# Kernel optimization log

Measured on AMD Instinct MI355X. Metric: run time of the kernel, lower is better.

Reference implementation:

```python
import jax, jax.numpy as jnp
import numpy as np

B, S, H, HEAD = 4, 4096, 512, 128
GAMMA = 0.96875
SCALE_BASE = 512  # XPOS default scale_base


def rotate_every_two(x):
    # (..., d) -> interleave (-x2, x1) pairs, matching torch stack+flatten
    x1 = x[..., ::2]
    x2 = x[..., 1::2]
    return jnp.stack((-x2, x1), axis=-1).reshape(x.shape)


def duplicate_interleave(m):
    # (L, d/2) -> (L, d): each column repeated twice, interleaved
    return jnp.repeat(m, 2, axis=-1)


def xpos(x, downscale=False):
    # x: (B, L, d). Faithful to XPOS module with offset=0.
    L, d = x.shape[1], x.shape[2]
    half = d // 2
    base_scale = (jnp.arange(0, d, 2, dtype=jnp.float32) + 0.4 * d) / (1.4 * d)  # (half,)
    power = jnp.arange(L, dtype=jnp.float32)[:, None] / SCALE_BASE              # (L,1)
    scale = base_scale[None, :] ** power                                        # (L,half)
    inv_freq = 1.0 / (10000.0 ** (jnp.arange(half, dtype=jnp.float32) / half))  # (half,)
    sinusoid = jnp.arange(L, dtype=jnp.float32)[:, None] * inv_freq[None, :]    # (L,half)
    sin, cos = jnp.sin(sinusoid), jnp.cos(sinusoid)
    if downscale:
        scale = 1.0 / scale
    sin = duplicate_interleave(sin * scale)  # (L,d)
    cos = duplicate_interleave(cos * scale)  # (L,d)
    return x * cos[None] + rotate_every_two(x) * sin[None]


def decay_mask(s1, s2, gamma):
    n = jnp.arange(s1)[:, None]
    m = jnp.arange(s2)[None, :]
    keep = n >= m
    # guard exponent to avoid inf for n<m (original zeroes NaNs from inf*0)
    exp = jnp.where(keep, (n - m).astype(jnp.float32), 0.0)
    return jnp.where(keep, gamma ** exp, 0.0)  # (s1,s2)


def setup_inputs() -> dict:
    key = jax.random.key(0)
    k1, k2, k3, k4, k5 = jax.random.split(key, 5)
    return {
        "X": jax.random.normal(k1, (B, S, H), dtype=jnp.float32),
        "Mem": jax.random.normal(k2, (B, S, H), dtype=jnp.float32),
        "W_Q": jax.random.normal(k3, (H, HEAD), dtype=jnp.float32) / H,
        "W_K": jax.random.normal(k4, (H, HEAD), dtype=jnp.float32) / H,
        "W_V": jax.random.normal(k5, (H, HEAD), dtype=jnp.float32) / H,
    }


def reference(X, Mem, W_Q, W_K, W_V):
    s1, s2 = X.shape[1], Mem.shape[1]
    D = decay_mask(s1, s2, GAMMA)                 # (s1,s2)
    Q = xpos(X @ W_Q)                              # (B,s1,head)
    K = xpos(Mem @ W_K, downscale=True)            # (B,s2,head)
    V = Mem @ W_V                                  # (B,s2,v)
    ret = jnp.einsum("bnd,bmd->bnm", Q, K) * D[None]  # (B,s1,s2)
    return ret @ V                                 # (B,s1,v)
```

## Files before the change

### kernel.cpp

```cpp
#include <hip/hip_runtime.h>
#include <hip/hip_bf16.h>

#define S_LEN 4096
#define HID   512
#define HD    128
#define LOG2_GAMMA (-0.0458036933f)

typedef short bf16x8 __attribute__((ext_vector_type(8)));
typedef float f32x4  __attribute__((ext_vector_type(4)));
typedef unsigned short u16;

static __device__ __forceinline__ u16 f2bf(float f) {
    union { float f; unsigned u; } v; v.f = f;
    unsigned r = (v.u + 0x7fffu + ((v.u >> 16) & 1u)) >> 16;
    return (u16)r;
}

static __device__ __forceinline__ unsigned pk2(float lo, float hi) {
    __hip_bfloat162 h = __float22bfloat162_rn(make_float2(lo, hi));
    union { __hip_bfloat162 h; unsigned u; } c; c.h = h; return c.u;
}
static __device__ __forceinline__ bf16x8 pack8(float4 a, float4 b) {
    union { unsigned u[4]; bf16x8 v; } r;
    r.u[0] = pk2(a.x, a.y); r.u[1] = pk2(a.z, a.w);
    r.u[2] = pk2(b.x, b.y); r.u[3] = pk2(b.z, b.w);
    return r.v;
}

static __device__ __forceinline__ void gload16(const void* g, void* l) {
    __builtin_amdgcn_global_load_lds(
        (const __attribute__((address_space(1))) unsigned*)g,
        (__attribute__((address_space(3))) unsigned*)l, 16, 0, 0);
}

__global__ __launch_bounds__(256) void prep_kernel(const float* __restrict__ WQ,
                                                   const float* __restrict__ WK,
                                                   const float* __restrict__ WV,
                                                   u16* __restrict__ Wt,
                                                   float2* __restrict__ tabQ,
                                                   float2* __restrict__ tabK) {
    if (blockIdx.x < 1024) {
        int idx = blockIdx.x * 256 + threadIdx.x;
        int n = idx >> 6, i = idx & 63;
        float base  = (2.0f * i + 51.2f) * (1.0f / 179.2f);
        float power = (float)n * (1.0f / 512.0f);
        float scale = exp2f(power * log2f(base));
        float inv_freq = exp2f(-(float)i * (13.287712379549449f / 64.0f));
        float theta = (float)n * inv_freq;
        float s, c;
        sincosf(theta, &s, &c);
        tabQ[idx] = make_float2(c * scale, s * scale);
        float is = 1.0f / scale;
        tabK[idx] = make_float2(c * is, s * is);
    } else {
        int idx = (blockIdx.x - 1024) * 256 + threadIdx.x;
        int w = idx >> 16;
        int rem = idx & 65535;
        int c = rem >> 9, k = rem & 511;
        const float* src = (w == 0) ? WQ : (w == 1) ? WK : WV;
        Wt[idx] = f2bf(src[k * HD + c]);
    }
}

__global__ __launch_bounds__(256) void proj_kernel(const float* __restrict__ X,
                                                   const float* __restrict__ Mem,
                                                   const u16* __restrict__ Wt,
                                                   const float2* __restrict__ tabQ,
                                                   const float2* __restrict__ tabK,
                                                   u16* __restrict__ Qo,
                                                   u16* __restrict__ Ko,
                                                   u16* __restrict__ Vt) {
    __shared__ __align__(16) float A_lds[2][2048];
    __shared__ __align__(16) u16   B_lds[2][2][4096];
    const int tid  = threadIdx.x;
    const int wave = tid >> 6, lane = tid & 63;
    const int l15  = lane & 15, quad = lane >> 4;
    const int rt_base = blockIdx.x * 64;

    if (blockIdx.y == 0) {
        auto stage = [&](int ch, int p) {
            const int kc0 = ch * 32;
#pragma unroll
            for (int i = 0; i < 2; ++i) {
                int L = i * 256 + tid;
                int row = L >> 3;
                int s = (L & 7) ^ (row & 7);
                gload16(X + (size_t)(rt_base + row) * HID + kc0 + s * 4,
                        &A_lds[p][(i * 256 + wave * 64) * 4]);
            }
#pragma unroll
            for (int i = 0; i < 2; ++i) {
                int L = i * 256 + tid;
                int col = L >> 2;
                int s = (L & 3) ^ ((col >> 1) & 3);
                gload16(Wt + (size_t)col * HID + kc0 + s * 8,
                        &B_lds[p][0][(i * 256 + wave * 64) * 8]);
            }
        };

        f32x4 acc[8];
#pragma unroll
        for (int ct = 0; ct < 8; ++ct) acc[ct] = (f32x4){0.f, 0.f, 0.f, 0.f};

        stage(0, 0);
        for (int ch = 0; ch < 16; ++ch) {
            const int p = ch & 1;
            __syncthreads();
            if (ch < 15) stage(ch + 1, p ^ 1);
            const int arow = wave * 16 + l15;
            float4 af0 = *(const float4*)&A_lds[p][(arow * 8 + ((quad * 2    ) ^ (l15 & 7))) * 4];
            float4 af1 = *(const float4*)&A_lds[p][(arow * 8 + ((quad * 2 + 1) ^ (l15 & 7))) * 4];
            bf16x8 a = pack8(af0, af1);
#pragma unroll
            for (int ct = 0; ct < 8; ++ct) {
                const int bu = (ct * 16 + l15) * 4 + (quad ^ ((l15 >> 1) & 3));
                bf16x8 b0 = *(const bf16x8*)&B_lds[p][0][bu * 8];
                acc[ct] = __builtin_amdgcn_mfma_f32_16x16x32_bf16(a, b0, acc[ct], 0, 0, 0);
            }
        }

#pragma unroll
        for (int ct = 0; ct < 8; ++ct) {
            int j = ct * 16 + l15;
            int i = j >> 1;
            float sgn = (j & 1) ? 1.0f : -1.0f;
#pragma unroll
            for (int r = 0; r < 4; ++r) {
                int t = rt_base + wave * 16 + quad * 4 + r;
                int n = t & 4095;
                float2 cs = tabQ[n * 64 + i];
                float v = acc[ct][r];
                float partner = __shfl_xor(v, 1, 64);
                Qo[(size_t)t * HD + j] = f2bf(v * cs.x + sgn * partner * cs.y);
            }
        }
    } else {
        const u16* WK_ = Wt + 65536;
        const u16* WV_ = Wt + 131072;

        auto stage = [&](int ch, int p) {
            const int kc0 = ch * 32;
#pragma unroll
            for (int i = 0; i < 2; ++i) {
                int L = i * 256 + tid;
                int row = L >> 3;
                int s = (L & 7) ^ (row & 7);
                gload16(Mem + (size_t)(rt_base + row) * HID + kc0 + s * 4,
                        &A_lds[p][(i * 256 + wave * 64) * 4]);
            }
#pragma unroll
            for (int i = 0; i < 2; ++i) {
                int L = i * 256 + tid;
                int col = L >> 2;
                int s = (L & 3) ^ ((col >> 1) & 3);
                gload16(WK_ + (size_t)col * HID + kc0 + s * 8,
                        &B_lds[p][0][(i * 256 + wave * 64) * 8]);
            }
#pragma unroll
            for (int i = 0; i < 2; ++i) {
                int L = i * 256 + tid;
                int col = L >> 2;
                int s = (L & 3) ^ ((col >> 1) & 3);
                gload16(WV_ + (size_t)col * HID + kc0 + s * 8,
                        &B_lds[p][1][(i * 256 + wave * 64) * 8]);
            }
        };

        f32x4 acc0[8], acc1[8];
#pragma unroll
        for (int ct = 0; ct < 8; ++ct) {
            acc0[ct] = (f32x4){0.f, 0.f, 0.f, 0.f};
            acc1[ct] = (f32x4){0.f, 0.f, 0.f, 0.f};
        }

        stage(0, 0);
        for (int ch = 0; ch < 16; ++ch) {
            const int p = ch & 1;
            __syncthreads();
            if (ch < 15) stage(ch + 1, p ^ 1);
            const int arow = wave * 16 + l15;
            float4 af0 = *(const float4*)&A_lds[p][(arow * 8 + ((quad * 2    ) ^ (l15 & 7))) * 4];
            float4 af1 = *(const float4*)&A_lds[p][(arow * 8 + ((quad * 2 + 1) ^ (l15 & 7))) * 4];
            bf16x8 a = pack8(af0, af1);
#pragma unroll
            for (int ct = 0; ct < 8; ++ct) {
                const int bu = (ct * 16 + l15) * 4 + (quad ^ ((l15 >> 1) & 3));
                bf16x8 b0 = *(const bf16x8*)&B_lds[p][0][bu * 8];
                bf16x8 b1 = *(const bf16x8*)&B_lds[p][1][bu * 8];
                acc0[ct] = __builtin_amdgcn_mfma_f32_16x16x32_bf16(a, b0, acc0[ct], 0, 0, 0);
                acc1[ct] = __builtin_amdgcn_mfma_f32_16x16x32_bf16(a, b1, acc1[ct], 0, 0, 0);
            }
        }

#pragma unroll
        for (int ct = 0; ct < 8; ++ct) {
            int j = ct * 16 + l15;
            int i = j >> 1;
            float sgn = (j & 1) ? 1.0f : -1.0f;
#pragma unroll
            for (int r = 0; r < 4; ++r) {
                int t = rt_base + wave * 16 + quad * 4 + r;
                int n = t & 4095;
                float2 cs = tabK[n * 64 + i];
                float v = acc0[ct][r];
                float partner = __shfl_xor(v, 1, 64);
                Ko[(size_t)t * HD + j] = f2bf(v * cs.x + sgn * partner * cs.y);
            }
        }

        u16* Vs = (u16*)&B_lds[0][0][0];
        __syncthreads();
#pragma unroll
        for (int ct = 0; ct < 8; ++ct) {
            int col = ct * 16 + l15;
#pragma unroll
            for (int r = 0; r < 4; ++r)
                Vs[col * 80 + wave * 16 + quad * 4 + r] = f2bf(acc1[ct][r]);
        }
        __syncthreads();
        int b = rt_base >> 12, sb = rt_base & 4095;
        int h = tid >> 1, sof = (tid & 1) * 32;
#pragma unroll
        for (int pp = 0; pp < 4; ++pp) {
            bf16x8 v = *(const bf16x8*)&Vs[h * 80 + sof + pp * 8];
            *(bf16x8*)(Vt + (size_t)(b * 128 + h) * S_LEN + sb + sof + pp * 8) = v;
        }
    }
}

__global__ __launch_bounds__(256) void ret_kernel(const u16* __restrict__ Qb,
                                                  const u16* __restrict__ Kb,
                                                  const u16* __restrict__ Vt,
                                                  float* __restrict__ out) {
    __shared__ __align__(16) u16   K_lds[2][8192];
    __shared__ __align__(16) float P_lds[4][16][68];
    const int tid  = threadIdx.x;
    const int wave = tid >> 6, lane = tid & 63;
    const int l15  = lane & 15, quad = lane >> 4;
    const int b  = blockIdx.x >> 6;
    const int qt = (blockIdx.x & 63) * 64;
    const int qw = qt + wave * 16;

    auto stageK = [&](int kv0, int p) {
#pragma unroll
        for (int i = 0; i < 4; ++i) {
            int u = i * 256 + tid;
            int kvr = u >> 4;
            int s = (u & 15) ^ (kvr & 15);
            gload16(Kb + (size_t)(b * S_LEN + kv0 + kvr) * HD + s * 8,
                    &K_lds[p][(i * 256 + wave * 64) * 8]);
        }
    };

    const size_t tq = (size_t)(b * S_LEN + qw + l15);
    bf16x8 qfrag[4];
#pragma unroll
    for (int kc = 0; kc < 4; ++kc)
        qfrag[kc] = *(const bf16x8*)(Qb + tq * HD + kc * 32 + quad * 8);

    f32x4 acco[8];
#pragma unroll
    for (int ht = 0; ht < 8; ++ht) acco[ht] = (f32x4){0.f, 0.f, 0.f, 0.f};

    int kv_lo = qt - 448; if (kv_lo < 0) kv_lo = 0;
    const int nt = (qt + 64 - kv_lo) >> 6;

    stageK(kv_lo, 0);
    for (int it = 0; it < nt; ++it) {
        const int p = it & 1;
        const int kv0 = kv_lo + it * 64;
        __syncthreads();
        if (it + 1 < nt) stageK(kv0 + 64, p ^ 1);

        bf16x8 vf[8][2];
#pragma unroll
        for (int ht = 0; ht < 8; ++ht) {
            const u16* vb = Vt + (size_t)(b * HD + ht * 16 + l15) * S_LEN + kv0 + quad * 8;
            vf[ht][0] = *(const bf16x8*)vb;
            vf[ht][1] = *(const bf16x8*)(vb + 32);
        }

        f32x4 accs[4];
#pragma unroll
        for (int ct = 0; ct < 4; ++ct) accs[ct] = (f32x4){0.f, 0.f, 0.f, 0.f};
#pragma unroll
        for (int ct = 0; ct < 4; ++ct) {
            const int kvr = ct * 16 + l15;
#pragma unroll
            for (int kc = 0; kc < 4; ++kc) {
                bf16x8 kf = *(const bf16x8*)
                    &K_lds[p][(kvr * 16 + ((kc * 4 + quad) ^ (kvr & 15))) * 8];
                accs[ct] = __builtin_amdgcn_mfma_f32_16x16x32_bf16(qfrag[kc], kf, accs[ct], 0, 0, 0);
            }
        }
#pragma unroll
        for (int ct = 0; ct < 4; ++ct) {
            int kvi = kv0 + ct * 16 + l15;
#pragma unroll
            for (int r = 0; r < 4; ++r) {
                int d = (qw + quad * 4 + r) - kvi;
                float w = exp2f((float)d * LOG2_GAMMA);
                P_lds[wave][quad * 4 + r][ct * 16 + l15] = (d >= 0) ? accs[ct][r] * w : 0.0f;
            }
        }
        float4 p00 = *(const float4*)&P_lds[wave][l15][quad * 8];
        float4 p01 = *(const float4*)&P_lds[wave][l15][quad * 8 + 4];
        float4 p10 = *(const float4*)&P_lds[wave][l15][32 + quad * 8];
        float4 p11 = *(const float4*)&P_lds[wave][l15][32 + quad * 8 + 4];
        bf16x8 pa0 = pack8(p00, p01);
        bf16x8 pa1 = pack8(p10, p11);
#pragma unroll
        for (int ht = 0; ht < 8; ++ht) {
            acco[ht] = __builtin_amdgcn_mfma_f32_16x16x32_bf16(pa0, vf[ht][0], acco[ht], 0, 0, 0);
            acco[ht] = __builtin_amdgcn_mfma_f32_16x16x32_bf16(pa1, vf[ht][1], acco[ht], 0, 0, 0);
        }
    }

#pragma unroll
    for (int ht = 0; ht < 8; ++ht)
#pragma unroll
        for (int r = 0; r < 4; ++r)
            out[(size_t)(b * S_LEN + qw + quad * 4 + r) * HD + ht * 16 + l15] = acco[ht][r];
}

extern "C" void kernel_launch(void* const* d_in, const int* in_sizes, int n_in,
                              void* d_out, int out_size, void* d_ws, size_t ws_size,
                              hipStream_t stream) {
    const float* X   = (const float*)d_in[0];
    const float* Mem = (const float*)d_in[1];
    const float* WQ  = (const float*)d_in[2];
    const float* WK  = (const float*)d_in[3];
    const float* WV  = (const float*)d_in[4];
    float* out = (float*)d_out;

    char* ws = (char*)d_ws;
    u16*    Qb   = (u16*)(ws);
    u16*    Kb   = (u16*)(ws + ((size_t)4 << 20));
    u16*    Vt   = (u16*)(ws + ((size_t)8 << 20));
    u16*    Wt   = (u16*)(ws + ((size_t)12 << 20));
    float2* tabQ = (float2*)(ws + ((size_t)13 << 20));
    float2* tabK = (float2*)(ws + ((size_t)15 << 20));

    prep_kernel<<<dim3(1792), dim3(256), 0, stream>>>(WQ, WK, WV, Wt, tabQ, tabK);
    proj_kernel<<<dim3(256, 2), dim3(256), 0, stream>>>(X, Mem, Wt, tabQ, tabK, Qb, Kb, Vt);
    ret_kernel<<<dim3(256), dim3(256), 0, stream>>>(Qb, Kb, Vt, out);
}
```

Before: 144.4 us.

## Split retention kernel into 32-row tiles with head-dim halves across waves

The retention kernel now launches twice as many blocks, each covering 32 query rows instead of 64. The four waves split into two row tiles times two halves of the value head dimension. Each wave keeps only half the output accumulators and V fragments, which raises parallelism and lowers register pressure. In exchange, the QK^T MFMAs and the decay masking are computed twice per row tile, and the K tiles are staged by twice as many blocks, with the KV window start aligned down to 64.

New measurement: 143.1 us. Within noise of the previous version (-0.9%).

```diff
diff --git a/kernel.cpp b/kernel.cpp
--- a/kernel.cpp
+++ b/kernel.cpp
@@ -237,9 +237,11 @@
     const int tid  = threadIdx.x;
     const int wave = tid >> 6, lane = tid & 63;
     const int l15  = lane & 15, quad = lane >> 4;
-    const int b  = blockIdx.x >> 6;
-    const int qt = (blockIdx.x & 63) * 64;
-    const int qw = qt + wave * 16;
+    const int b  = blockIdx.x >> 7;
+    const int qt = (blockIdx.x & 127) * 32;
+    const int rt = wave & 1;
+    const int hh = wave >> 1;
+    const int qw = qt + rt * 16;
 
     auto stageK = [&](int kv0, int p) {
 #pragma unroll
@@ -258,12 +260,14 @@
     for (int kc = 0; kc < 4; ++kc)
         qfrag[kc] = *(const bf16x8*)(Qb + tq * HD + kc * 32 + quad * 8);
 
-    f32x4 acco[8];
-#pragma unroll
-    for (int ht = 0; ht < 8; ++ht) acco[ht] = (f32x4){0.f, 0.f, 0.f, 0.f};
-
-    int kv_lo = qt - 448; if (kv_lo < 0) kv_lo = 0;
-    const int nt = (qt + 64 - kv_lo) >> 6;
+    f32x4 acco[4];
+#pragma unroll
+    for (int hc = 0; hc < 4; ++hc) acco[hc] = (f32x4){0.f, 0.f, 0.f, 0.f};
+
+    int kv_lo = qt - 448;
+    kv_lo &= ~63;
+    if (kv_lo < 0) kv_lo = 0;
+    const int nt = (qt + 32 - kv_lo + 63) >> 6;
 
     stageK(kv_lo, 0);
     for (int it = 0; it < nt; ++it) {
@@ -272,12 +276,13 @@
         __syncthreads();
         if (it + 1 < nt) stageK(kv0 + 64, p ^ 1);
 
-        bf16x8 vf[8][2];
-#pragma unroll
-        for (int ht = 0; ht < 8; ++ht) {
-            const u16* vb = Vt + (size_t)(b * HD + ht * 16 + l15) * S_LEN + kv0 + quad * 8;
-            vf[ht][0] = *(const bf16x8*)vb;
-            vf[ht][1] = *(const bf16x8*)(vb + 32);
+        bf16x8 vf[4][2];
+#pragma unroll
+        for (int hc = 0; hc < 4; ++hc) {
+            const u16* vb = Vt + (size_t)(b * HD + (hh * 4 + hc) * 16 + l15) * S_LEN
+                            + kv0 + quad * 8;
+            vf[hc][0] = *(const bf16x8*)vb;
+            vf[hc][1] = *(const bf16x8*)(vb + 32);
         }
 
         f32x4 accs[4];
@@ -310,17 +315,18 @@
         bf16x8 pa0 = pack8(p00, p01);
         bf16x8 pa1 = pack8(p10, p11);
 #pragma unroll
-        for (int ht = 0; ht < 8; ++ht) {
-            acco[ht] = __builtin_amdgcn_mfma_f32_16x16x32_bf16(pa0, vf[ht][0], acco[ht], 0, 0, 0);
-            acco[ht] = __builtin_amdgcn_mfma_f32_16x16x32_bf16(pa1, vf[ht][1], acco[ht], 0, 0, 0);
+        for (int hc = 0; hc < 4; ++hc) {
+            acco[hc] = __builtin_amdgcn_mfma_f32_16x16x32_bf16(pa0, vf[hc][0], acco[hc], 0, 0, 0);
+            acco[hc] = __builtin_amdgcn_mfma_f32_16x16x32_bf16(pa1, vf[hc][1], acco[hc], 0, 0, 0);
         }
     }
 
 #pragma unroll
-    for (int ht = 0; ht < 8; ++ht)
+    for (int hc = 0; hc < 4; ++hc)
 #pragma unroll
         for (int r = 0; r < 4; ++r)
-            out[(size_t)(b * S_LEN + qw + quad * 4 + r) * HD + ht * 16 + l15] = acco[ht][r];
+            out[(size_t)(b * S_LEN + qw + quad * 4 + r) * HD + hh * 64 + hc * 16 + l15]
+                = acco[hc][r];
 }
 
 extern "C" void kernel_launch(void* const* d_in, const int* in_sizes, int n_in,
@@ -343,5 +349,5 @@
 
     prep_kernel<<<dim3(1792), dim3(256), 0, stream>>>(WQ, WK, WV, Wt, tabQ, tabK);
     proj_kernel<<<dim3(256, 2), dim3(256), 0, stream>>>(X, Mem, Wt, tabQ, tabK, Qb, Kb, Vt);
-    ret_kernel<<<dim3(256), dim3(256), 0, stream>>>(Qb, Kb, Vt, out);
-}
+    ret_kernel<<<dim3(512), dim3(256), 0, stream>>>(Qb, Kb, Vt, out);
+}
```
